# Kernel tuning notes

Measured on AMD Instinct MI355X. Metric: run time of the kernel, lower is better.

The kernel has to match this reference:

```python
import jax, jax.numpy as jnp
import numpy as np

B, NL, EL, D, H = 16, 512, 1024, 256, 8
HD = D // H
EPS = 1e-5


def _layernorm(x, g, b):
    mu = jnp.mean(x, axis=-1, keepdims=True)
    var = jnp.mean(jnp.square(x - mu), axis=-1, keepdims=True)
    return (x - mu) * jax.lax.rsqrt(var + EPS) * g + b


def setup_inputs() -> dict:
    key = jax.random.key(0)
    ks = jax.random.split(key, 12)
    # xavier-uniform-ish scale for projections
    def xavier(k, shape):
        fan_in, fan_out = shape[0], shape[1]
        lim = float(np.sqrt(6.0 / (fan_in + fan_out)))
        return jax.random.uniform(k, shape, jnp.float32, -lim, lim)
    return {
        "node_x": jax.random.normal(ks[0], (B, NL, D), jnp.float32),
        "edge_x": jax.random.normal(ks[1], (B, EL, D), jnp.float32),
        "node_mask": jnp.zeros((B, NL, NL + EL), dtype=bool),
        "W1": xavier(ks[2], (D, 3 * D)),
        "b1": jnp.zeros((3 * D,), jnp.float32),
        "W2": xavier(ks[3], (D, 2 * D)),
        "b2": jnp.zeros((2 * D,), jnp.float32),
        "lin1_w": xavier(ks[4], (D, D)),
        "lin1_b": jnp.zeros((D,), jnp.float32),
        "lin2_w": xavier(ks[5], (D, D)),
        "lin2_b": jnp.zeros((D,), jnp.float32),
        "ln1_g": jnp.ones((D,), jnp.float32),
        "ln1_b": jnp.zeros((D,), jnp.float32),
        "ln2_g": jnp.ones((D,), jnp.float32),
        "ln2_b": jnp.zeros((D,), jnp.float32),
    }


def reference(node_x, edge_x, node_mask, W1, b1, W2, b2,
              lin1_w, lin1_b, lin2_w, lin2_b, ln1_g, ln1_b, ln2_g, ln2_b):
    b, nl, d = node_x.shape
    el = edge_x.shape[1]
    scaling = float(HD) ** -0.5
    # projections (batch-first; equivalent to the seq-first torch code)
    qkv = node_x @ W1 + b1                       # [b, nl, 3d]
    q, k_node, v_node = jnp.split(qkv, 3, axis=-1)
    kv_e = edge_x @ W2 + b2                      # [b, el, 2d]
    k_edge, v_edge = jnp.split(kv_e, 2, axis=-1)
    k = jnp.concatenate([k_node, k_edge], axis=1)  # [b, nl+el, d]
    v = jnp.concatenate([v_node, v_edge], axis=1)
    # split heads
    qh = q.reshape(b, nl, H, HD)
    kh = k.reshape(b, nl + el, H, HD)
    vh = v.reshape(b, nl + el, H, HD)
    scores = jnp.einsum('bqhd,bkhd->bhqk', qh, kh) * scaling  # [b,h,nl,nl+el]
    scores = jnp.where(node_mask[:, None, :, :], -jnp.inf, scores)
    attn = jax.nn.softmax(scores, axis=-1)
    ctx = jnp.einsum('bhqk,bkhd->bqhd', attn, vh).reshape(b, nl, d)
    # residual + LN1 (dropout is identity in eval/p=0)
    x = _layernorm(node_x + ctx, ln1_g, ln1_b)
    # FFN (relu) + residual + LN2; torch Linear: y = x @ W.T + b
    ff = jax.nn.relu(x @ lin1_w.T + lin1_b) @ lin2_w.T + lin2_b
    x = _layernorm(x + ff, ln2_g, ln2_b)
    return x
```

## Files before the change

kernel.cpp:

```cpp
#include <hip/hip_runtime.h>
#include <hip/hip_bf16.h>

using u16 = unsigned short;
using u32 = unsigned int;
using u64 = unsigned long long;
typedef __attribute__((ext_vector_type(8))) short short8;
typedef __attribute__((ext_vector_type(4))) float f32x4;
typedef __attribute__((ext_vector_type(16))) float f32x16;
typedef __attribute__((ext_vector_type(4))) u32 u32x4;

constexpr int kB = 16, kNL = 512, kEL = 1024, kD = 256, kH = 8, kHD = 32;
constexpr int kS = kNL + kEL;
constexpr int kM1 = kB * kNL;
constexpr float kScale = 0.17677669529663687f;
constexpr float kLog2e = 1.4426950408889634f;
constexpr float kQS = kScale * kLog2e;
constexpr float kEps = 1e-5f;

__device__ __forceinline__ u16 f2bh(float f) {
    __hip_bfloat16 h = __float2bfloat16(f);
    return __builtin_bit_cast(u16, h);
}
__device__ __forceinline__ u32 packbf(float lo, float hi) {
    return (__float_as_uint(hi) & 0xffff0000u) | (__float_as_uint(lo) >> 16);
}
__device__ __forceinline__ void load4(const float* p, float* o) {
    float4 v = *reinterpret_cast<const float4*>(p);
    o[0] = v.x; o[1] = v.y; o[2] = v.z; o[3] = v.w;
}
__device__ __forceinline__ f32x16 fzero16() {
    f32x16 z;
    #pragma unroll
    for (int i = 0; i < 16; ++i) z[i] = 0.f;
    return z;
}

__global__ __launch_bounds__(256) void prep_k(
    const float* __restrict__ W1, const float* __restrict__ W2,
    const float* __restrict__ l1w, const float* __restrict__ l2w,
    const float* __restrict__ nodef, const float* __restrict__ edgef,
    const u32* __restrict__ mask,
    u16* __restrict__ Wt1, u16* __restrict__ Wt2,
    u16* __restrict__ Wt3, u16* __restrict__ Wt4,
    u16* __restrict__ nodeb, u16* __restrict__ edgeb,
    u32* __restrict__ Mw)
{
    const int sec = blockIdx.y, bid = blockIdx.x, t = threadIdx.x;
    if (sec == 6) {
        if (bid >= 2048) return;
        const int row = bid * 4 + (t >> 6);
        const int l = t & 63;
        const u32* mr = mask + (size_t)row * (kS / 4);
        u32 word = 0;
        #pragma unroll
        for (int k = 0; k < 6; ++k) {
            const u32 v = mr[k * 64 + l];
            const u64 bal = __ballot(v != 0);
            word |= (((bal) & 0xffffull) ? 1u : 0u) << (k * 4 + 0);
            word |= (((bal >> 16) & 0xffffull) ? 1u : 0u) << (k * 4 + 1);
            word |= (((bal >> 32) & 0xffffull) ? 1u : 0u) << (k * 4 + 2);
            word |= (((bal >> 48) & 0xffffull) ? 1u : 0u) << (k * 4 + 3);
        }
        if (l == 0) Mw[row] = word;
        return;
    }
    if (sec >= 4) {
        const float* src = (sec == 4) ? nodef : edgef;
        u16* dst = (sec == 4) ? nodeb : edgeb;
        const int nblk = (sec == 4) ? 2048 : 4096;
        if (bid >= nblk) return;
        const int i = bid * 1024 + t * 4;
        float v[4]; load4(src + i, v);
        ushort4 o = {f2bh(v[0]), f2bh(v[1]), f2bh(v[2]), f2bh(v[3])};
        *reinterpret_cast<ushort4*>(dst + i) = o;
        return;
    }
    if (sec >= 2) {
        if (bid >= 64) return;
        const float* src = (sec == 2) ? l1w : l2w;
        u16* dst = (sec == 2) ? Wt3 : Wt4;
        const int i = bid * 1024 + t * 4;
        float v[4]; load4(src + i, v);
        ushort4 o = {f2bh(v[0]), f2bh(v[1]), f2bh(v[2]), f2bh(v[3])};
        *reinterpret_cast<ushort4*>(dst + i) = o;
        return;
    }
    const int N = (sec == 0) ? 768 : 512;
    if (bid >= 8 * (N / 32)) return;
    const float* src = (sec == 0) ? W1 : W2;
    u16* dst = (sec == 0) ? Wt1 : Wt2;
    const int tk = bid / (N / 32), tn = bid % (N / 32);
    __shared__ float T[32][33];
    {
        const int k = t >> 3, n4 = (t & 7) * 4;
        float v[4]; load4(src + (size_t)(tk * 32 + k) * N + tn * 32 + n4, v);
        T[n4+0][k] = v[0]; T[n4+1][k] = v[1]; T[n4+2][k] = v[2]; T[n4+3][k] = v[3];
    }
    __syncthreads();
    {
        const int n = t >> 3, k4 = (t & 7) * 4;
        ushort4 o = {f2bh(T[n][k4+0]), f2bh(T[n][k4+1]),
                     f2bh(T[n][k4+2]), f2bh(T[n][k4+3])};
        *reinterpret_cast<ushort4*>(dst + (size_t)(tn*32 + n) * 256 + tk*32 + k4) = o;
    }
}

template<int BM, int BN, int N, int K, int MODE>
__global__ __launch_bounds__(256) void gemm_mfma(
    const u16* __restrict__ A, const u16* __restrict__ Wt,
    const float* __restrict__ bias,
    void* __restrict__ o0v, void* __restrict__ o1v, void* __restrict__ o2v)
{
    constexpr int MI = (BM / 2) / 16;
    constexpr int NI = (BN / 2) / 16;
    __shared__ u16 AsB[2][BM * 40];
    __shared__ u16 BsB[2][BN * 40];
    const int t = threadIdx.x;
    const int w = t >> 6, l = t & 63;
    const int wr = w >> 1, wc = w & 1;
    const int lq = l & 15, lg = l >> 4;
    const int bm = blockIdx.x * BM, bn = blockIdx.y * BN;

    f32x4 acc[MI][NI];
    #pragma unroll
    for (int mi = 0; mi < MI; ++mi)
        #pragma unroll
        for (int ni = 0; ni < NI; ++ni) acc[mi][ni] = (f32x4){0.f, 0.f, 0.f, 0.f};

    auto stage = [&](int buf, int kk) {
        u16* As = AsB[buf];
        u16* Bs = BsB[buf];
        if constexpr (BM == 128) {
            const int m = t >> 1, kh = (t & 1) * 16;
            const u16* ap = A + (size_t)(bm + m) * K + kk + kh;
            *reinterpret_cast<short8*>(&As[m * 40 + kh]) =
                *reinterpret_cast<const short8*>(ap);
            *reinterpret_cast<short8*>(&As[m * 40 + kh + 8]) =
                *reinterpret_cast<const short8*>(ap + 8);
        } else {
            const int m = t >> 2, kq = (t & 3) * 8;
            *reinterpret_cast<short8*>(&As[m * 40 + kq]) =
                *reinterpret_cast<const short8*>(A + (size_t)(bm + m) * K + kk + kq);
        }
        if constexpr (BN == 128) {
            const int n = t >> 1, kh = (t & 1) * 16;
            const u16* bp = Wt + (size_t)(bn + n) * K + kk + kh;
            *reinterpret_cast<short8*>(&Bs[n * 40 + kh]) =
                *reinterpret_cast<const short8*>(bp);
            *reinterpret_cast<short8*>(&Bs[n * 40 + kh + 8]) =
                *reinterpret_cast<const short8*>(bp + 8);
        } else {
            const int n = t >> 2, kq = (t & 3) * 8;
            *reinterpret_cast<short8*>(&Bs[n * 40 + kq]) =
                *reinterpret_cast<const short8*>(Wt + (size_t)(bn + n) * K + kk + kq);
        }
    };

    stage(0, 0);
    __syncthreads();
    int buf = 0;
    for (int kk = 0; kk < K; kk += 32) {
        if (kk + 32 < K) stage(buf ^ 1, kk + 32);
        const u16* As = AsB[buf];
        const u16* Bs = BsB[buf];
        short8 bf[NI];
        #pragma unroll
        for (int ni = 0; ni < NI; ++ni)
            bf[ni] = *reinterpret_cast<const short8*>(
                &Bs[(wc * (BN / 2) + ni * 16 + lq) * 40 + lg * 8]);
        #pragma unroll
        for (int mi = 0; mi < MI; ++mi) {
            const short8 af = *reinterpret_cast<const short8*>(
                &As[(wr * (BM / 2) + mi * 16 + lq) * 40 + lg * 8]);
            #pragma unroll
            for (int ni = 0; ni < NI; ++ni)
                acc[mi][ni] = __builtin_amdgcn_mfma_f32_16x16x32_bf16(
                    af, bf[ni], acc[mi][ni], 0, 0, 0);
        }
        __syncthreads();
        buf ^= 1;
    }

    #pragma unroll
    for (int mi = 0; mi < MI; ++mi) {
        #pragma unroll
        for (int ni = 0; ni < NI; ++ni) {
            const int cg = bn + wc * (BN / 2) + ni * 16 + lq;
            const int rg0 = bm + wr * (BM / 2) + mi * 16 + lg * 4;
            const float bv = bias[cg];
            float y[4];
            #pragma unroll
            for (int r = 0; r < 4; ++r) {
                y[r] = acc[mi][ni][r] + bv;
                if (MODE == 2) y[r] = fmaxf(y[r], 0.f);
            }
            if constexpr (MODE == 0) {
                u16* qo = (u16*)o0v; u16* ko = (u16*)o1v; u16* vt = (u16*)o2v;
                const int bidx = rg0 >> 9, key = rg0 & 511;
                if (cg < 256) {
                    #pragma unroll
                    for (int r = 0; r < 4; ++r)
                        qo[(size_t)(rg0 + r) * kD + cg] = f2bh(y[r] * kQS);
                } else if (cg < 512) {
                    #pragma unroll
                    for (int r = 0; r < 4; ++r)
                        ko[((size_t)bidx * kS + key + r) * kD + (cg - 256)] = f2bh(y[r]);
                } else {
                    const int d0 = cg - 512, hh = d0 >> 5, dd = d0 & 31;
                    ushort4 o = {f2bh(y[0]), f2bh(y[1]), f2bh(y[2]), f2bh(y[3])};
                    *reinterpret_cast<ushort4*>(
                        vt + ((size_t)(bidx * kH + hh) * kHD + dd) * kS + key) = o;
                }
            } else if constexpr (MODE == 1) {
                u16* ko = (u16*)o0v; u16* vt = (u16*)o1v;
                const int bidx = rg0 >> 10, key = kNL + (rg0 & 1023);
                if (cg < 256) {
                    #pragma unroll
                    for (int r = 0; r < 4; ++r)
                        ko[((size_t)bidx * kS + key + r) * kD + cg] = f2bh(y[r]);
                } else {
                    const int d0 = cg - 256, hh = d0 >> 5, dd = d0 & 31;
                    ushort4 o = {f2bh(y[0]), f2bh(y[1]), f2bh(y[2]), f2bh(y[3])};
                    *reinterpret_cast<ushort4*>(
                        vt + ((size_t)(bidx * kH + hh) * kHD + dd) * kS + key) = o;
                }
            } else if constexpr (MODE == 2) {
                u16* o0 = (u16*)o0v;
                #pragma unroll
                for (int r = 0; r < 4; ++r)
                    o0[(size_t)(rg0 + r) * N + cg] = f2bh(y[r]);
            } else {
                float* o0 = (float*)o0v;
                #pragma unroll
                for (int r = 0; r < 4; ++r)
                    o0[(size_t)(rg0 + r) * N + cg] = y[r];
            }
        }
    }
}

__global__ __launch_bounds__(256) void attn_mfma(
    const u16* __restrict__ Qb, const u16* __restrict__ Kb,
    const u16* __restrict__ VTb, const unsigned char* __restrict__ mask,
    const u32* __restrict__ Mw, float* __restrict__ O)
{
    __shared__ float mba[4][64][17];
    __shared__ float mbb[4][64][17];
    const int t = threadIdx.x;
    const int w = t >> 6, l = t & 63;
    const int q32 = l & 31, hi = l >> 5;
    const int bid = blockIdx.x;
    const int h = bid & 7;
    const int qt = (bid >> 3) & 7;
    const int b = bid >> 6;
    const int qra = qt * 64 + q32;
    const int qrb = qra + 32;

    const u16* qpa = Qb + ((size_t)(b * kNL) + qra) * kD + h * kHD;
    const u16* qpb = Qb + ((size_t)(b * kNL) + qrb) * kD + h * kHD;
    const short8 qf0a = *reinterpret_cast<const short8*>(qpa + hi * 8);
    const short8 qf1a = *reinterpret_cast<const short8*>(qpa + 16 + hi * 8);
    const short8 qf0b = *reinterpret_cast<const short8*>(qpb + hi * 8);
    const short8 qf1b = *reinterpret_cast<const short8*>(qpb + 16 + hi * 8);

    const u16* kbase  = Kb  + ((size_t)b * kS) * kD + h * kHD;
    const u16* vtbase = VTb + ((size_t)(b * kH + h) * kHD) * kS;
    const unsigned char* mra = mask + ((size_t)(b * kNL) + qra) * kS;
    const unsigned char* mrb = mask + ((size_t)(b * kNL) + qrb) * kS;
    const u32 mbitsa = Mw[b * kNL + qra];
    const u32 mbitsb = Mw[b * kNL + qrb];

    f32x16 acca = fzero16(), accb = fzero16();
    float la = 0.f, lb = 0.f;

#define HALFG(kfA, kfB, vfA, vfB, keyh, QF0, QF1, ACC, LRUN, COLD, MROW) do {  \
        f32x16 s = __builtin_amdgcn_mfma_f32_32x32x16_bf16(kfA, QF0, fzero16(), 0, 0, 0); \
        s = __builtin_amdgcn_mfma_f32_32x32x16_bf16(kfB, QF1, s, 0, 0, 0);     \
        float e[16];                                                           \
        _Pragma("unroll")                                                      \
        for (int n = 0; n < 16; ++n) e[n] = __builtin_amdgcn_exp2f(s[n]);      \
        if (COLD) {                                                            \
            _Pragma("unroll")                                                  \
            for (int n = 0; n < 16; ++n) {                                     \
                const int key = (keyh) + (n & 3) + 8 * (n >> 2) + 4 * hi;      \
                if (MROW[key]) e[n] = 0.f;                                     \
            }                                                                  \
        }                                                                      \
        u32 pk[8];                                                             \
        _Pragma("unroll")                                                      \
        for (int qd = 0; qd < 4; ++qd) {                                       \
            LRUN += (e[4*qd] + e[4*qd+1]) + (e[4*qd+2] + e[4*qd+3]);           \
            pk[2*qd]   = packbf(e[4*qd],   e[4*qd+1]);                         \
            pk[2*qd+1] = packbf(e[4*qd+2], e[4*qd+3]);                         \
        }                                                                      \
        {                                                                      \
            u32 xa = pk[0], ya = pk[2], xb = pk[1], yb = pk[3];                \
            asm("v_permlane32_swap_b32 %0, %1" : "+v"(xa), "+v"(ya));          \
            asm("v_permlane32_swap_b32 %0, %1" : "+v"(xb), "+v"(yb));          \
            const short8 pb = __builtin_bit_cast(short8, (u32x4){xa, xb, ya, yb}); \
            __builtin_amdgcn_s_setprio(1);                                     \
            ACC = __builtin_amdgcn_mfma_f32_32x32x16_bf16(vfA, pb, ACC, 0, 0, 0); \
            __builtin_amdgcn_s_setprio(0);                                     \
        }                                                                      \
        {                                                                      \
            u32 xa = pk[4], ya = pk[6], xb = pk[5], yb = pk[7];                \
            asm("v_permlane32_swap_b32 %0, %1" : "+v"(xa), "+v"(ya));          \
            asm("v_permlane32_swap_b32 %0, %1" : "+v"(xb), "+v"(yb));          \
            const short8 pb = __builtin_bit_cast(short8, (u32x4){xa, xb, ya, yb}); \
            __builtin_amdgcn_s_setprio(1);                                     \
            ACC = __builtin_amdgcn_mfma_f32_32x32x16_bf16(vfB, pb, ACC, 0, 0, 0); \
            __builtin_amdgcn_s_setprio(0);                                     \
        }                                                                      \
} while (0)

    const int ktBeg = w * 6, ktEnd = ktBeg + 6;
    for (int kt = ktBeg; kt < ktEnd; ++kt) {
        const int key0 = kt * 64;
        const u16* krow = kbase + (size_t)(key0 + q32) * kD + hi * 8;
        const u16* vrow = vtbase + (size_t)q32 * kS + key0 + hi * 8;
        const short8 a0 = *reinterpret_cast<const short8*>(krow);
        const short8 a1 = *reinterpret_cast<const short8*>(krow + 16);
        const short8 a2 = *reinterpret_cast<const short8*>(krow + 32 * kD);
        const short8 a3 = *reinterpret_cast<const short8*>(krow + 32 * kD + 16);
        const short8 v0 = *reinterpret_cast<const short8*>(vrow);
        const short8 v1 = *reinterpret_cast<const short8*>(vrow + 16);
        const short8 v2 = *reinterpret_cast<const short8*>(vrow + 32);
        const short8 v3 = *reinterpret_cast<const short8*>(vrow + 48);
        const bool colda = __any(((mbitsa >> kt) & 1u) != 0u);
        const bool coldb = __any(((mbitsb >> kt) & 1u) != 0u);
        HALFG(a0, a1, v0, v1, key0, qf0a, qf1a, acca, la, colda, mra);
        HALFG(a0, a1, v0, v1, key0, qf0b, qf1b, accb, lb, coldb, mrb);
        HALFG(a2, a3, v2, v3, key0 + 32, qf0a, qf1a, acca, la, colda, mra);
        HALFG(a2, a3, v2, v3, key0 + 32, qf0b, qf1b, accb, lb, coldb, mrb);
    }
#undef HALFG

    la += __shfl_xor(la, 32);
    lb += __shfl_xor(lb, 32);

    mba[w][l][0] = la;
    mbb[w][l][0] = lb;
    #pragma unroll
    for (int j = 0; j < 16; ++j) { mba[w][l][1 + j] = acca[j]; mbb[w][l][1 + j] = accb[j]; }
    __syncthreads();
    if (w == 0) {
        {
            float lt = la;
            float ov[16];
            #pragma unroll
            for (int i = 0; i < 16; ++i) ov[i] = acca[i];
            #pragma unroll
            for (int j = 1; j < 4; ++j) {
                lt += mba[j][l][0];
                #pragma unroll
                for (int i = 0; i < 16; ++i) ov[i] += mba[j][l][1 + i];
            }
            const float inv = (lt > 0.f) ? 1.f / lt : 0.f;
            float* orow = O + ((size_t)(b * kNL) + qra) * kD + h * kHD;
            #pragma unroll
            for (int qd = 0; qd < 4; ++qd) {
                float4 o = {ov[4*qd+0] * inv, ov[4*qd+1] * inv,
                            ov[4*qd+2] * inv, ov[4*qd+3] * inv};
                *reinterpret_cast<float4*>(orow + qd * 8 + 4 * hi) = o;
            }
        }
        {
            float lt = lb;
            float ov[16];
            #pragma unroll
            for (int i = 0; i < 16; ++i) ov[i] = accb[i];
            #pragma unroll
            for (int j = 1; j < 4; ++j) {
                lt += mbb[j][l][0];
                #pragma unroll
                for (int i = 0; i < 16; ++i) ov[i] += mbb[j][l][1 + i];
            }
            const float inv = (lt > 0.f) ? 1.f / lt : 0.f;
            float* orow = O + ((size_t)(b * kNL) + qrb) * kD + h * kHD;
            #pragma unroll
            for (int qd = 0; qd < 4; ++qd) {
                float4 o = {ov[4*qd+0] * inv, ov[4*qd+1] * inv,
                            ov[4*qd+2] * inv, ov[4*qd+3] * inv};
                *reinterpret_cast<float4*>(orow + qd * 8 + 4 * hi) = o;
            }
        }
    }
}

template<bool DUAL>
__global__ __launch_bounds__(256) void ln_k(
    const float* __restrict__ a_, const float* __restrict__ r,
    const float* __restrict__ gam, const float* __restrict__ bet,
    float* __restrict__ out_, u16* __restrict__ outh)
{
    const int row = blockIdx.x * 4 + (threadIdx.x >> 6);
    const int lane = threadIdx.x & 63;
    const size_t base = (size_t)row * kD + lane * 4;
    float xv[4];
    load4(a_ + base, xv);
    float rv[4];
    load4(r + base, rv);
    #pragma unroll
    for (int t = 0; t < 4; ++t) xv[t] += rv[t];
    float s = xv[0] + xv[1] + xv[2] + xv[3];
    float q = xv[0]*xv[0] + xv[1]*xv[1] + xv[2]*xv[2] + xv[3]*xv[3];
    #pragma unroll
    for (int off = 1; off < 64; off <<= 1) {
        s += __shfl_xor(s, off);
        q += __shfl_xor(q, off);
    }
    const float mean = s * (1.0f / kD);
    const float var = q * (1.0f / kD) - mean * mean;
    const float rs = rsqrtf(var + kEps);
    float gv[4], bv[4];
    load4(gam + lane * 4, gv);
    load4(bet + lane * 4, bv);
    float y[4];
    #pragma unroll
    for (int t = 0; t < 4; ++t) y[t] = (xv[t] - mean) * rs * gv[t] + bv[t];
    float4 o = {y[0], y[1], y[2], y[3]};
    *reinterpret_cast<float4*>(out_ + base) = o;
    if constexpr (DUAL) {
        ushort4 ob = {f2bh(y[0]), f2bh(y[1]), f2bh(y[2]), f2bh(y[3])};
        *reinterpret_cast<ushort4*>(outh + base) = ob;
    }
}

extern "C" void kernel_launch(void* const* d_in, const int* in_sizes, int n_in,
                              void* d_out, int out_size, void* d_ws, size_t ws_size,
                              hipStream_t stream)
{
    const float* node_x = (const float*)d_in[0];
    const float* edge_x = (const float*)d_in[1];
    const unsigned char* mask = (const unsigned char*)d_in[2];
    const float* W1  = (const float*)d_in[3];
    const float* b1  = (const float*)d_in[4];
    const float* W2  = (const float*)d_in[5];
    const float* b2  = (const float*)d_in[6];
    const float* l1w = (const float*)d_in[7];
    const float* l1b = (const float*)d_in[8];
    const float* l2w = (const float*)d_in[9];
    const float* l2b = (const float*)d_in[10];
    const float* g1  = (const float*)d_in[11];
    const float* be1 = (const float*)d_in[12];
    const float* g2  = (const float*)d_in[13];
    const float* be2 = (const float*)d_in[14];

    char* w = (char*)d_ws;
    u16*   qb  = (u16*)(w);
    u16*   wt1 = (u16*)(w + (4u<<20));
    u16*   wt2 = (u16*)(w + (4u<<20) + 393216);
    u16*   wt3 = (u16*)(w + (4u<<20) + 655360);
    u16*   wt4 = (u16*)(w + (4u<<20) + 786432);
    u32*   mw  = (u32*)(w + (4u<<20) + 917504);
    u16*   nxb = (u16*)(w + (5u<<20));
    u16*   exb = (u16*)(w + (9u<<20));
    u16*   kb  = (u16*)(w + (17u<<20));
    u16*   vt  = (u16*)(w + (30u<<20));
    float* cx  = (float*)(w + (43u<<20));
    float* xb  = (float*)(w + (52u<<20));
    u16*   xbh = exb;
    u16*   fh  = qb;

    prep_k<<<dim3(4096, 7), 256, 0, stream>>>(
        W1, W2, l1w, l2w, node_x, edge_x, (const u32*)mask,
        wt1, wt2, wt3, wt4, nxb, exb, mw);
    gemm_mfma<128, 128, 768, 256, 0><<<dim3(kM1 / 128, 6), 256, 0, stream>>>(
        nxb, wt1, b1, qb, kb, vt);
    gemm_mfma<128, 128, 512, 256, 1><<<dim3(kB * kEL / 128, 4), 256, 0, stream>>>(
        exb, wt2, b2, kb, vt, nullptr);
    attn_mfma<<<kB * kH * 8, 256, 0, stream>>>(qb, kb, vt, mask, mw, cx);
    ln_k<true><<<kM1 / 4, 256, 0, stream>>>(node_x, cx, g1, be1, xb, xbh);
    gemm_mfma<64, 128, 256, 256, 2><<<dim3(kM1 / 64, 2), 256, 0, stream>>>(
        xbh, wt3, l1b, fh, nullptr, nullptr);
    gemm_mfma<64, 128, 256, 256, 3><<<dim3(kM1 / 64, 2), 256, 0, stream>>>(
        fh, wt4, l2b, cx, nullptr, nullptr);
    ln_k<false><<<kM1 / 4, 256, 0, stream>>>(xb, cx, g2, be2, (float*)d_out, nullptr);
}
```

Baseline: 99.62 us.

## Merge QKV projection launches and fuse FFN2 with LayerNorm2

Runs the node QKV GEMM and the edge KV GEMM as one launch with a block-index split. It also fuses the second FFN GEMM with the residual add and LayerNorm2: each block computes a full 32-row by 256-column output tile, stages it in shared memory and normalises it in place. This removes two kernel launches and the fp32 round trip of the FFN output through global memory. In exchange, FFN2 runs on fewer, larger blocks with a 32-row tile, which may lower occupancy and MFMA efficiency.

```diff
diff --git a/kernel.cpp b/kernel.cpp
--- a/kernel.cpp
+++ b/kernel.cpp
@@ -105,55 +105,35 @@
     }
 }
 
-template<int BM, int BN, int N, int K, int MODE>
-__global__ __launch_bounds__(256) void gemm_mfma(
+template<int N, int K, int MODE>
+__device__ __forceinline__ void gemm_body128(
     const u16* __restrict__ A, const u16* __restrict__ Wt,
     const float* __restrict__ bias,
-    void* __restrict__ o0v, void* __restrict__ o1v, void* __restrict__ o2v)
-{
-    constexpr int MI = (BM / 2) / 16;
-    constexpr int NI = (BN / 2) / 16;
-    __shared__ u16 AsB[2][BM * 40];
-    __shared__ u16 BsB[2][BN * 40];
+    void* __restrict__ o0v, void* __restrict__ o1v, void* __restrict__ o2v,
+    int bx, int by, u16* AsB, u16* BsB)
+{
     const int t = threadIdx.x;
     const int w = t >> 6, l = t & 63;
     const int wr = w >> 1, wc = w & 1;
     const int lq = l & 15, lg = l >> 4;
-    const int bm = blockIdx.x * BM, bn = blockIdx.y * BN;
-
-    f32x4 acc[MI][NI];
-    #pragma unroll
-    for (int mi = 0; mi < MI; ++mi)
-        #pragma unroll
-        for (int ni = 0; ni < NI; ++ni) acc[mi][ni] = (f32x4){0.f, 0.f, 0.f, 0.f};
+    const int bm = bx * 128, bn = by * 128;
+
+    f32x4 acc[4][4];
+    #pragma unroll
+    for (int mi = 0; mi < 4; ++mi)
+        #pragma unroll
+        for (int ni = 0; ni < 4; ++ni) acc[mi][ni] = (f32x4){0.f, 0.f, 0.f, 0.f};
 
     auto stage = [&](int buf, int kk) {
-        u16* As = AsB[buf];
-        u16* Bs = BsB[buf];
-        if constexpr (BM == 128) {
-            const int m = t >> 1, kh = (t & 1) * 16;
-            const u16* ap = A + (size_t)(bm + m) * K + kk + kh;
-            *reinterpret_cast<short8*>(&As[m * 40 + kh]) =
-                *reinterpret_cast<const short8*>(ap);
-            *reinterpret_cast<short8*>(&As[m * 40 + kh + 8]) =
-                *reinterpret_cast<const short8*>(ap + 8);
-        } else {
-            const int m = t >> 2, kq = (t & 3) * 8;
-            *reinterpret_cast<short8*>(&As[m * 40 + kq]) =
-                *reinterpret_cast<const short8*>(A + (size_t)(bm + m) * K + kk + kq);
-        }
-        if constexpr (BN == 128) {
-            const int n = t >> 1, kh = (t & 1) * 16;
-            const u16* bp = Wt + (size_t)(bn + n) * K + kk + kh;
-            *reinterpret_cast<short8*>(&Bs[n * 40 + kh]) =
-                *reinterpret_cast<const short8*>(bp);
-            *reinterpret_cast<short8*>(&Bs[n * 40 + kh + 8]) =
-                *reinterpret_cast<const short8*>(bp + 8);
-        } else {
-            const int n = t >> 2, kq = (t & 3) * 8;
-            *reinterpret_cast<short8*>(&Bs[n * 40 + kq]) =
-                *reinterpret_cast<const short8*>(Wt + (size_t)(bn + n) * K + kk + kq);
-        }
+        u16* As = AsB + buf * (128 * 40);
+        u16* Bs = BsB + buf * (128 * 40);
+        const int m = t >> 1, kh = (t & 1) * 16;
+        const u16* ap = A + (size_t)(bm + m) * K + kk + kh;
+        *reinterpret_cast<short8*>(&As[m * 40 + kh]) = *reinterpret_cast<const short8*>(ap);
+        *reinterpret_cast<short8*>(&As[m * 40 + kh + 8]) = *reinterpret_cast<const short8*>(ap + 8);
+        const u16* bp = Wt + (size_t)(bn + m) * K + kk + kh;
+        *reinterpret_cast<short8*>(&Bs[m * 40 + kh]) = *reinterpret_cast<const short8*>(bp);
+        *reinterpret_cast<short8*>(&Bs[m * 40 + kh + 8]) = *reinterpret_cast<const short8*>(bp + 8);
     };
 
     stage(0, 0);
@@ -161,19 +141,19 @@
     int buf = 0;
     for (int kk = 0; kk < K; kk += 32) {
         if (kk + 32 < K) stage(buf ^ 1, kk + 32);
-        const u16* As = AsB[buf];
-        const u16* Bs = BsB[buf];
-        short8 bf[NI];
-        #pragma unroll
-        for (int ni = 0; ni < NI; ++ni)
+        const u16* As = AsB + buf * (128 * 40);
+        const u16* Bs = BsB + buf * (128 * 40);
+        short8 bf[4];
+        #pragma unroll
+        for (int ni = 0; ni < 4; ++ni)
             bf[ni] = *reinterpret_cast<const short8*>(
-                &Bs[(wc * (BN / 2) + ni * 16 + lq) * 40 + lg * 8]);
-        #pragma unroll
-        for (int mi = 0; mi < MI; ++mi) {
+                &Bs[(wc * 64 + ni * 16 + lq) * 40 + lg * 8]);
+        #pragma unroll
+        for (int mi = 0; mi < 4; ++mi) {
             const short8 af = *reinterpret_cast<const short8*>(
-                &As[(wr * (BM / 2) + mi * 16 + lq) * 40 + lg * 8]);
-            #pragma unroll
-            for (int ni = 0; ni < NI; ++ni)
+                &As[(wr * 64 + mi * 16 + lq) * 40 + lg * 8]);
+            #pragma unroll
+            for (int ni = 0; ni < 4; ++ni)
                 acc[mi][ni] = __builtin_amdgcn_mfma_f32_16x16x32_bf16(
                     af, bf[ni], acc[mi][ni], 0, 0, 0);
         }
@@ -182,18 +162,15 @@
     }
 
     #pragma unroll
-    for (int mi = 0; mi < MI; ++mi) {
-        #pragma unroll
-        for (int ni = 0; ni < NI; ++ni) {
-            const int cg = bn + wc * (BN / 2) + ni * 16 + lq;
-            const int rg0 = bm + wr * (BM / 2) + mi * 16 + lg * 4;
+    for (int mi = 0; mi < 4; ++mi) {
+        #pragma unroll
+        for (int ni = 0; ni < 4; ++ni) {
+            const int cg = bn + wc * 64 + ni * 16 + lq;
+            const int rg0 = bm + wr * 64 + mi * 16 + lg * 4;
             const float bv = bias[cg];
             float y[4];
             #pragma unroll
-            for (int r = 0; r < 4; ++r) {
-                y[r] = acc[mi][ni][r] + bv;
-                if (MODE == 2) y[r] = fmaxf(y[r], 0.f);
-            }
+            for (int r = 0; r < 4; ++r) y[r] = acc[mi][ni][r] + bv;
             if constexpr (MODE == 0) {
                 u16* qo = (u16*)o0v; u16* ko = (u16*)o1v; u16* vt = (u16*)o2v;
                 const int bidx = rg0 >> 9, key = rg0 & 511;
@@ -211,7 +188,7 @@
                     *reinterpret_cast<ushort4*>(
                         vt + ((size_t)(bidx * kH + hh) * kHD + dd) * kS + key) = o;
                 }
-            } else if constexpr (MODE == 1) {
+            } else {
                 u16* ko = (u16*)o0v; u16* vt = (u16*)o1v;
                 const int bidx = rg0 >> 10, key = kNL + (rg0 & 1023);
                 if (cg < 256) {
@@ -224,18 +201,199 @@
                     *reinterpret_cast<ushort4*>(
                         vt + ((size_t)(bidx * kH + hh) * kHD + dd) * kS + key) = o;
                 }
-            } else if constexpr (MODE == 2) {
-                u16* o0 = (u16*)o0v;
-                #pragma unroll
-                for (int r = 0; r < 4; ++r)
-                    o0[(size_t)(rg0 + r) * N + cg] = f2bh(y[r]);
-            } else {
-                float* o0 = (float*)o0v;
-                #pragma unroll
-                for (int r = 0; r < 4; ++r)
-                    o0[(size_t)(rg0 + r) * N + cg] = y[r];
             }
         }
+    }
+}
+
+__global__ __launch_bounds__(256) void qkv_both(
+    const u16* __restrict__ nxb, const u16* __restrict__ exb,
+    const u16* __restrict__ wt1, const u16* __restrict__ wt2,
+    const float* __restrict__ b1, const float* __restrict__ b2,
+    u16* __restrict__ qb, u16* __restrict__ kb, u16* __restrict__ vt)
+{
+    __shared__ u16 AsB[2 * 128 * 40];
+    __shared__ u16 BsB[2 * 128 * 40];
+    const int bid = blockIdx.x;
+    if (bid < 384) {
+        gemm_body128<768, 256, 0>(nxb, wt1, b1, qb, kb, vt,
+                                  bid & 63, bid >> 6, AsB, BsB);
+    } else {
+        const int r = bid - 384;
+        gemm_body128<512, 256, 1>(exb, wt2, b2, kb, vt, nullptr,
+                                  r & 127, r >> 7, AsB, BsB);
+    }
+}
+
+__global__ __launch_bounds__(256) void ffn1_k(
+    const u16* __restrict__ A, const u16* __restrict__ Wt,
+    const float* __restrict__ bias, u16* __restrict__ out)
+{
+    __shared__ u16 AsB[2][64 * 40];
+    __shared__ u16 BsB[2][128 * 40];
+    const int t = threadIdx.x;
+    const int w = t >> 6, l = t & 63;
+    const int wr = w >> 1, wc = w & 1;
+    const int lq = l & 15, lg = l >> 4;
+    const int bm = blockIdx.x * 64, bn = blockIdx.y * 128;
+    constexpr int K = 256;
+
+    f32x4 acc[2][4];
+    #pragma unroll
+    for (int mi = 0; mi < 2; ++mi)
+        #pragma unroll
+        for (int ni = 0; ni < 4; ++ni) acc[mi][ni] = (f32x4){0.f, 0.f, 0.f, 0.f};
+
+    auto stage = [&](int buf, int kk) {
+        {
+            const int m = t >> 2, kq = (t & 3) * 8;
+            *reinterpret_cast<short8*>(&AsB[buf][m * 40 + kq]) =
+                *reinterpret_cast<const short8*>(A + (size_t)(bm + m) * K + kk + kq);
+        }
+        {
+            const int n = t >> 1, kh = (t & 1) * 16;
+            const u16* bp = Wt + (size_t)(bn + n) * K + kk + kh;
+            *reinterpret_cast<short8*>(&BsB[buf][n * 40 + kh]) =
+                *reinterpret_cast<const short8*>(bp);
+            *reinterpret_cast<short8*>(&BsB[buf][n * 40 + kh + 8]) =
+                *reinterpret_cast<const short8*>(bp + 8);
+        }
+    };
+
+    stage(0, 0);
+    __syncthreads();
+    int buf = 0;
+    for (int kk = 0; kk < K; kk += 32) {
+        if (kk + 32 < K) stage(buf ^ 1, kk + 32);
+        short8 bf[4];
+        #pragma unroll
+        for (int ni = 0; ni < 4; ++ni)
+            bf[ni] = *reinterpret_cast<const short8*>(
+                &BsB[buf][(wc * 64 + ni * 16 + lq) * 40 + lg * 8]);
+        #pragma unroll
+        for (int mi = 0; mi < 2; ++mi) {
+            const short8 af = *reinterpret_cast<const short8*>(
+                &AsB[buf][(wr * 32 + mi * 16 + lq) * 40 + lg * 8]);
+            #pragma unroll
+            for (int ni = 0; ni < 4; ++ni)
+                acc[mi][ni] = __builtin_amdgcn_mfma_f32_16x16x32_bf16(
+                    af, bf[ni], acc[mi][ni], 0, 0, 0);
+        }
+        __syncthreads();
+        buf ^= 1;
+    }
+
+    #pragma unroll
+    for (int mi = 0; mi < 2; ++mi) {
+        #pragma unroll
+        for (int ni = 0; ni < 4; ++ni) {
+            const int cg = bn + wc * 64 + ni * 16 + lq;
+            const int rg0 = bm + wr * 32 + mi * 16 + lg * 4;
+            const float bv = bias[cg];
+            #pragma unroll
+            for (int r = 0; r < 4; ++r)
+                out[(size_t)(rg0 + r) * 256 + cg] = f2bh(fmaxf(acc[mi][ni][r] + bv, 0.f));
+        }
+    }
+}
+
+__global__ __launch_bounds__(256) void ffn2_ln2_k(
+    const u16* __restrict__ A, const u16* __restrict__ Wt,
+    const float* __restrict__ bias, const float* __restrict__ xb,
+    const float* __restrict__ gam, const float* __restrict__ bet,
+    float* __restrict__ out)
+{
+    __shared__ __align__(16) char smem[46080];
+    u16* AsB = (u16*)smem;
+    u16* BsB = (u16*)(smem + 2 * 32 * 40 * 2);
+    float* lnb = (float*)smem;
+    const int t = threadIdx.x;
+    const int w = t >> 6, l = t & 63;
+    const int wr = w >> 1, wc = w & 1;
+    const int lq = l & 15, lg = l >> 4;
+    const int bm = blockIdx.x * 32;
+    constexpr int K = 256;
+
+    f32x4 acc[8];
+    #pragma unroll
+    for (int ni = 0; ni < 8; ++ni) acc[ni] = (f32x4){0.f, 0.f, 0.f, 0.f};
+
+    auto stage = [&](int buf, int kk) {
+        {
+            const int m = t >> 3, kq = (t & 7) * 4;
+            *reinterpret_cast<ushort4*>(&AsB[buf * 32 * 40 + m * 40 + kq]) =
+                *reinterpret_cast<const ushort4*>(A + (size_t)(bm + m) * K + kk + kq);
+        }
+        {
+            const int n = t;
+            const u16* bp = Wt + (size_t)n * K + kk;
+            u16* dst = &BsB[buf * 256 * 40 + n * 40];
+            #pragma unroll
+            for (int j = 0; j < 4; ++j)
+                *reinterpret_cast<short8*>(dst + j * 8) =
+                    *reinterpret_cast<const short8*>(bp + j * 8);
+        }
+    };
+
+    stage(0, 0);
+    __syncthreads();
+    int buf = 0;
+    for (int kk = 0; kk < K; kk += 32) {
+        if (kk + 32 < K) stage(buf ^ 1, kk + 32);
+        short8 bf[8];
+        #pragma unroll
+        for (int ni = 0; ni < 8; ++ni)
+            bf[ni] = *reinterpret_cast<const short8*>(
+                &BsB[buf * 256 * 40 + (wc * 128 + ni * 16 + lq) * 40 + lg * 8]);
+        const short8 af = *reinterpret_cast<const short8*>(
+            &AsB[buf * 32 * 40 + (wr * 16 + lq) * 40 + lg * 8]);
+        #pragma unroll
+        for (int ni = 0; ni < 8; ++ni)
+            acc[ni] = __builtin_amdgcn_mfma_f32_16x16x32_bf16(af, bf[ni], acc[ni], 0, 0, 0);
+        __syncthreads();
+        buf ^= 1;
+    }
+
+    #pragma unroll
+    for (int ni = 0; ni < 8; ++ni) {
+        const int cg = wc * 128 + ni * 16 + lq;
+        const int rl0 = wr * 16 + lg * 4;
+        const float bv = bias[cg];
+        #pragma unroll
+        for (int r = 0; r < 4; ++r)
+            lnb[(rl0 + r) * 260 + cg] = acc[ni][r] + bv;
+    }
+    __syncthreads();
+
+    #pragma unroll
+    for (int rr = 0; rr < 8; ++rr) {
+        const int rl = w * 8 + rr;
+        const int row = bm + rl;
+        float xv[4];
+        float4 yv = *reinterpret_cast<const float4*>(&lnb[rl * 260 + l * 4]);
+        float rv[4];
+        load4(xb + (size_t)row * kD + l * 4, rv);
+        xv[0] = yv.x + rv[0]; xv[1] = yv.y + rv[1];
+        xv[2] = yv.z + rv[2]; xv[3] = yv.w + rv[3];
+        float s = xv[0] + xv[1] + xv[2] + xv[3];
+        float q = xv[0]*xv[0] + xv[1]*xv[1] + xv[2]*xv[2] + xv[3]*xv[3];
+        #pragma unroll
+        for (int off = 1; off < 64; off <<= 1) {
+            s += __shfl_xor(s, off);
+            q += __shfl_xor(q, off);
+        }
+        const float mean = s * (1.0f / kD);
+        const float var = q * (1.0f / kD) - mean * mean;
+        const float rs = rsqrtf(var + kEps);
+        float gv[4], bv[4];
+        load4(gam + l * 4, gv);
+        load4(bet + l * 4, bv);
+        float4 o;
+        o.x = (xv[0] - mean) * rs * gv[0] + bv[0];
+        o.y = (xv[1] - mean) * rs * gv[1] + bv[1];
+        o.z = (xv[2] - mean) * rs * gv[2] + bv[2];
+        o.w = (xv[3] - mean) * rs * gv[3] + bv[3];
+        *reinterpret_cast<float4*>(out + (size_t)row * kD + l * 4) = o;
     }
 }
 
@@ -294,19 +452,19 @@
             pk[2*qd+1] = packbf(e[4*qd+2], e[4*qd+3]);                         \
         }                                                                      \
         {                                                                      \
-            u32 xa = pk[0], ya = pk[2], xb = pk[1], yb = pk[3];                \
+            u32 xa = pk[0], ya = pk[2], xb_ = pk[1], yb_ = pk[3];              \
             asm("v_permlane32_swap_b32 %0, %1" : "+v"(xa), "+v"(ya));          \
-            asm("v_permlane32_swap_b32 %0, %1" : "+v"(xb), "+v"(yb));          \
-            const short8 pb = __builtin_bit_cast(short8, (u32x4){xa, xb, ya, yb}); \
+            asm("v_permlane32_swap_b32 %0, %1" : "+v"(xb_), "+v"(yb_));        \
+            const short8 pb = __builtin_bit_cast(short8, (u32x4){xa, xb_, ya, yb_}); \
             __builtin_amdgcn_s_setprio(1);                                     \
             ACC = __builtin_amdgcn_mfma_f32_32x32x16_bf16(vfA, pb, ACC, 0, 0, 0); \
             __builtin_amdgcn_s_setprio(0);                                     \
         }                                                                      \
         {                                                                      \
-            u32 xa = pk[4], ya = pk[6], xb = pk[5], yb = pk[7];                \
+            u32 xa = pk[4], ya = pk[6], xb_ = pk[5], yb_ = pk[7];              \
             asm("v_permlane32_swap_b32 %0, %1" : "+v"(xa), "+v"(ya));          \
-            asm("v_permlane32_swap_b32 %0, %1" : "+v"(xb), "+v"(yb));          \
-            const short8 pb = __builtin_bit_cast(short8, (u32x4){xa, xb, ya, yb}); \
+            asm("v_permlane32_swap_b32 %0, %1" : "+v"(xb_), "+v"(yb_));        \
+            const short8 pb = __builtin_bit_cast(short8, (u32x4){xa, xb_, ya, yb_}); \
             __builtin_amdgcn_s_setprio(1);                                     \
             ACC = __builtin_amdgcn_mfma_f32_32x32x16_bf16(vfB, pb, ACC, 0, 0, 0); \
             __builtin_amdgcn_s_setprio(0);                                     \
@@ -465,15 +623,9 @@
     prep_k<<<dim3(4096, 7), 256, 0, stream>>>(
         W1, W2, l1w, l2w, node_x, edge_x, (const u32*)mask,
         wt1, wt2, wt3, wt4, nxb, exb, mw);
-    gemm_mfma<128, 128, 768, 256, 0><<<dim3(kM1 / 128, 6), 256, 0, stream>>>(
-        nxb, wt1, b1, qb, kb, vt);
-    gemm_mfma<128, 128, 512, 256, 1><<<dim3(kB * kEL / 128, 4), 256, 0, stream>>>(
-        exb, wt2, b2, kb, vt, nullptr);
+    qkv_both<<<896, 256, 0, stream>>>(nxb, exb, wt1, wt2, b1, b2, qb, kb, vt);
     attn_mfma<<<kB * kH * 8, 256, 0, stream>>>(qb, kb, vt, mask, mw, cx);
     ln_k<true><<<kM1 / 4, 256, 0, stream>>>(node_x, cx, g1, be1, xb, xbh);
-    gemm_mfma<64, 128, 256, 256, 2><<<dim3(kM1 / 64, 2), 256, 0, stream>>>(
-        xbh, wt3, l1b, fh, nullptr, nullptr);
-    gemm_mfma<64, 128, 256, 256, 3><<<dim3(kM1 / 64, 2), 256, 0, stream>>>(
-        fh, wt4, l2b, cx, nullptr, nullptr);
-    ln_k<false><<<kM1 / 4, 256, 0, stream>>>(xb, cx, g2, be2, (float*)d_out, nullptr);
-}
+    ffn1_k<<<dim3(kM1 / 64, 2), 256, 0, stream>>>(xbh, wt3, l1b, fh);
+    ffn2_ln2_k<<<kM1 / 32, 256, 0, stream>>>(fh, wt4, l2b, xb, g2, be2, (float*)d_out);
+}
```

New measurement: 95.24 us. 1.05x faster.
